# Kernel tuning notes

Hardware: AMD Instinct MI355X
Metric: run time of the kernel (lower is better)

The kernel has to match this reference:

```python
import jax, jax.numpy as jnp
import numpy as np

EPS = 1e-5

def setup_inputs() -> dict:
    key = jax.random.key(0)
    k1, k2 = jax.random.split(key)
    x = jax.random.normal(k1, (32, 256, 56, 56), dtype=jnp.float32)
    conv_w = jax.random.normal(k2, (1, 2, 5, 5), dtype=jnp.float32) * 0.1
    gamma = jnp.ones((1,), dtype=jnp.float32)
    beta = jnp.zeros((1,), dtype=jnp.float32)
    return {"x": x, "conv_w": conv_w, "gamma": gamma, "beta": beta}

def reference(x, conv_w, gamma, beta):
    # channel max and mean -> [N, 2, H, W]
    y = jnp.stack([jnp.max(x, axis=1), jnp.mean(x, axis=1)], axis=1)
    # 5x5 conv, 2->1 channels, SAME padding, no bias -> [N, 1, H, W]
    y = jax.lax.conv_general_dilated(
        y, conv_w, window_strides=(1, 1), padding=((2, 2), (2, 2)),
        dimension_numbers=("NCHW", "OIHW", "NCHW"))
    # BatchNorm2d(1) in training mode: batch statistics over (N, H, W)
    mean = jnp.mean(y, axis=(0, 2, 3), keepdims=True)
    var = jnp.mean(jnp.square(y - mean), axis=(0, 2, 3), keepdims=True)
    y = (y - mean) * jax.lax.rsqrt(var + EPS)
    y = y * gamma.reshape(1, -1, 1, 1) + beta.reshape(1, -1, 1, 1)
    # double sigmoid gate, broadcast over channels
    return x * jax.nn.sigmoid(jax.nn.sigmoid(y))
```

## Files before the change

kernel.cpp:

```cpp
#include <hip/hip_runtime.h>

#define NN 32
#define CC 256
#define HH 56
#define WW 56
#define HWSZ 3136
#define QPP 784
#define NQ 25088
#define NHW 100352
#define CBLKS 32
#define APPLY_THREADS (NQ * CBLKS)

typedef float v4f __attribute__((ext_vector_type(4)));

__device__ __forceinline__ float4 f4max(float4 a, float4 b) {
    float4 r;
    r.x = fmaxf(a.x, b.x); r.y = fmaxf(a.y, b.y);
    r.z = fmaxf(a.z, b.z); r.w = fmaxf(a.w, b.w);
    return r;
}
__device__ __forceinline__ float4 f4add(float4 a, float4 b) {
    float4 r;
    r.x = a.x + b.x; r.y = a.y + b.y; r.z = a.z + b.z; r.w = a.w + b.w;
    return r;
}

__global__ __launch_bounds__(256) void k_pool_part(const float* __restrict__ x,
                                                   float* __restrict__ pmaxp,
                                                   float* __restrict__ psump,
                                                   float* __restrict__ stats) {
    if (blockIdx.x == 0 && threadIdx.x == 0 && threadIdx.y == 0) {
        stats[0] = 0.f;
        stats[1] = 0.f;
    }
    const int tx = threadIdx.x;
    const int ty = threadIdx.y;
    const int tile = blockIdx.x >> 2;
    const int quarter = blockIdx.x & 3;
    const int qid = tile * 64 + tx;
    const int n = qid / QPP;
    const int hwq = qid - n * QPP;
    const int cbase = quarter * 64 + ty * 16;

    const float4* p = (const float4*)x + (size_t)(n * CC + cbase) * QPP + hwq;
    float4 v0 = p[0];
    float4 vmax = v0, vsum = v0;
#pragma unroll 8
    for (int i = 1; i < 16; ++i) {
        float4 v = p[(size_t)i * QPP];
        vmax = f4max(vmax, v);
        vsum = f4add(vsum, v);
    }
    __shared__ float4 smax[4][64];
    __shared__ float4 ssum[4][64];
    smax[ty][tx] = vmax;
    ssum[ty][tx] = vsum;
    __syncthreads();
    if (ty == 0) {
        float4 m = smax[0][tx];
        float4 s = ssum[0][tx];
#pragma unroll
        for (int g = 1; g < 4; ++g) {
            m = f4max(m, smax[g][tx]);
            s = f4add(s, ssum[g][tx]);
        }
        ((float4*)pmaxp)[(size_t)quarter * NQ + qid] = m;
        ((float4*)psump)[(size_t)quarter * NQ + qid] = s;
    }
}

__global__ __launch_bounds__(256) void k_merge(const float* __restrict__ pmaxp,
                                               const float* __restrict__ psump,
                                               float* __restrict__ pool) {
    const int q = blockIdx.x * 256 + threadIdx.x;
    if (q >= NQ) return;
    float4 m = ((const float4*)pmaxp)[q];
    float4 s = ((const float4*)psump)[q];
#pragma unroll
    for (int g = 1; g < 4; ++g) {
        m = f4max(m, ((const float4*)pmaxp)[(size_t)g * NQ + q]);
        s = f4add(s, ((const float4*)psump)[(size_t)g * NQ + q]);
    }
    const int n = q / QPP;
    const int hwq = q - n * QPP;
    ((float4*)pool)[(size_t)n * 2 * QPP + hwq] = m;
    float4 mean;
    mean.x = s.x * 0.00390625f; mean.y = s.y * 0.00390625f;
    mean.z = s.z * 0.00390625f; mean.w = s.w * 0.00390625f;
    ((float4*)pool)[(size_t)n * 2 * QPP + QPP + hwq] = mean;
}

__global__ __launch_bounds__(256) void k_conv(const float* __restrict__ pool,
                                              const float* __restrict__ cw,
                                              float* __restrict__ conv,
                                              float* __restrict__ stats) {
    __shared__ float w[50];
    const int tid = threadIdx.x;
    if (tid < 50) w[tid] = cw[tid];
    __syncthreads();

    const int gid = blockIdx.x * 256 + tid;
    const int n = gid / HWSZ;
    const int hw = gid - n * HWSZ;
    const int h = hw / WW;
    const int wc = hw - h * WW;

    const float* pb = pool + (size_t)n * 2 * HWSZ;
    float acc = 0.f;
#pragma unroll
    for (int ci = 0; ci < 2; ++ci)
#pragma unroll
        for (int kh = 0; kh < 5; ++kh) {
            const int hh = h + kh - 2;
            if (hh < 0 || hh >= HH) continue;
#pragma unroll
            for (int kw = 0; kw < 5; ++kw) {
                const int wwc = wc + kw - 2;
                if (wwc < 0 || wwc >= WW) continue;
                acc += pb[ci * HWSZ + hh * WW + wwc] * w[ci * 25 + kh * 5 + kw];
            }
        }
    conv[gid] = acc;

    float s = acc, s2 = acc * acc;
#pragma unroll
    for (int i = 1; i < 64; i <<= 1) {
        s += __shfl_xor(s, i);
        s2 += __shfl_xor(s2, i);
    }
    if ((tid & 63) == 0) {
        atomicAdd(&stats[0], s);
        atomicAdd(&stats[1], s2);
    }
}

__global__ __launch_bounds__(256) void k_apply(const float* __restrict__ x,
                                               const float* __restrict__ conv,
                                               const float* __restrict__ stats,
                                               const float* __restrict__ gamma,
                                               const float* __restrict__ beta,
                                               float* __restrict__ out) {
    const float invM = 1.f / (float)NHW;
    const float mean = stats[0] * invM;
    const float var = stats[1] * invM - mean * mean;
    const float scale = rsqrtf(var + 1e-5f) * gamma[0];
    const float shift = beta[0] - mean * scale;

    const int gid = blockIdx.x * 256 + threadIdx.x;
    const int v = gid / QPP;
    const int hwq = gid - v * QPP;
    const int cblk = v & (CBLKS - 1);
    const int n = v >> 5;

    const float4 cv = ((const float4*)conv)[n * QPP + hwq];
    float4 g;
    {
        float t = cv.x * scale + shift;
        float s1 = 1.f / (1.f + __expf(-t));
        g.x = 1.f / (1.f + __expf(-s1));
    }
    {
        float t = cv.y * scale + shift;
        float s1 = 1.f / (1.f + __expf(-t));
        g.y = 1.f / (1.f + __expf(-s1));
    }
    {
        float t = cv.z * scale + shift;
        float s1 = 1.f / (1.f + __expf(-t));
        g.z = 1.f / (1.f + __expf(-s1));
    }
    {
        float t = cv.w * scale + shift;
        float s1 = 1.f / (1.f + __expf(-t));
        g.w = 1.f / (1.f + __expf(-s1));
    }

    const float4* x4 = (const float4*)x + (size_t)(n * CC + cblk * 8) * QPP + hwq;
    v4f* o4 = (v4f*)out + (size_t)(n * CC + cblk * 8) * QPP + hwq;
#pragma unroll
    for (int i = 0; i < 8; ++i) {
        float4 xv = x4[(size_t)i * QPP];
        v4f r;
        r.x = xv.x * g.x; r.y = xv.y * g.y;
        r.z = xv.z * g.z; r.w = xv.w * g.w;
        __builtin_nontemporal_store(r, &o4[(size_t)i * QPP]);
    }
}

extern "C" void kernel_launch(void* const* d_in, const int* in_sizes, int n_in,
                              void* d_out, int out_size, void* d_ws, size_t ws_size,
                              hipStream_t stream) {
    const float* x = (const float*)d_in[0];
    const float* cw = (const float*)d_in[1];
    const float* gamma = (const float*)d_in[2];
    const float* beta = (const float*)d_in[3];
    float* out = (float*)d_out;

    float* ws = (float*)d_ws;
    float* pmaxp = ws;
    float* psump = pmaxp + (size_t)4 * NQ * 4;
    float* pool = psump + (size_t)4 * NQ * 4;
    float* conv = pool + 2 * NHW;
    float* stats = conv + NHW;

    k_pool_part<<<1568, dim3(64, 4), 0, stream>>>(x, pmaxp, psump, stats);
    k_merge<<<98, 256, 0, stream>>>(pmaxp, psump, pool);
    k_conv<<<392, 256, 0, stream>>>(pool, cw, conv, stats);
    k_apply<<<APPLY_THREADS / 256, 256, 0, stream>>>(x, conv, stats, gamma,
                                                     beta, out);
}
```

Baseline: 100.6 us.

## Drop shared-memory pool reduction; split channels into 8 groups of 32

The pooling kernel no longer does a shared-memory tree reduction. Each thread now reduces 32 channels straight to global partials, spread over 8 channel groups, and the merge kernel combines 8 partials instead of 4. The apply kernel gives each thread 32 channels instead of 8, so a quarter as many threads recompute the double-sigmoid gate. This cuts the LDS traffic, the barrier and the redundant gate math. The cost is fewer threads in flight, longer serial per-thread loops, and twice as many partial writes in the merge stage.

```diff
diff --git a/kernel.cpp b/kernel.cpp
--- a/kernel.cpp
+++ b/kernel.cpp
@@ -8,8 +8,9 @@
 #define QPP 784
 #define NQ 25088
 #define NHW 100352
-#define CBLKS 32
-#define APPLY_THREADS (NQ * CBLKS)
+#define NGRP 8
+#define CPGRP 32
+#define ABLK 8
 
 typedef float v4f __attribute__((ext_vector_type(4)));
 
@@ -25,48 +26,31 @@
     return r;
 }
 
-__global__ __launch_bounds__(256) void k_pool_part(const float* __restrict__ x,
-                                                   float* __restrict__ pmaxp,
-                                                   float* __restrict__ psump,
-                                                   float* __restrict__ stats) {
-    if (blockIdx.x == 0 && threadIdx.x == 0 && threadIdx.y == 0) {
+__global__ __launch_bounds__(256) void k_pool_lin(const float* __restrict__ x,
+                                                  float* __restrict__ pmaxp,
+                                                  float* __restrict__ psump,
+                                                  float* __restrict__ stats) {
+    if (blockIdx.x == 0 && threadIdx.x == 0) {
         stats[0] = 0.f;
         stats[1] = 0.f;
     }
-    const int tx = threadIdx.x;
-    const int ty = threadIdx.y;
-    const int tile = blockIdx.x >> 2;
-    const int quarter = blockIdx.x & 3;
-    const int qid = tile * 64 + tx;
-    const int n = qid / QPP;
-    const int hwq = qid - n * QPP;
-    const int cbase = quarter * 64 + ty * 16;
+    const int gid = blockIdx.x * 256 + threadIdx.x;
+    const int grp = gid / NQ;
+    const int r = gid - grp * NQ;
+    const int n = r / QPP;
+    const int hwq = r - n * QPP;
 
-    const float4* p = (const float4*)x + (size_t)(n * CC + cbase) * QPP + hwq;
+    const float4* p = (const float4*)x + (size_t)(n * CC + grp * CPGRP) * QPP + hwq;
     float4 v0 = p[0];
     float4 vmax = v0, vsum = v0;
 #pragma unroll 8
-    for (int i = 1; i < 16; ++i) {
+    for (int i = 1; i < CPGRP; ++i) {
         float4 v = p[(size_t)i * QPP];
         vmax = f4max(vmax, v);
         vsum = f4add(vsum, v);
     }
-    __shared__ float4 smax[4][64];
-    __shared__ float4 ssum[4][64];
-    smax[ty][tx] = vmax;
-    ssum[ty][tx] = vsum;
-    __syncthreads();
-    if (ty == 0) {
-        float4 m = smax[0][tx];
-        float4 s = ssum[0][tx];
-#pragma unroll
-        for (int g = 1; g < 4; ++g) {
-            m = f4max(m, smax[g][tx]);
-            s = f4add(s, ssum[g][tx]);
-        }
-        ((float4*)pmaxp)[(size_t)quarter * NQ + qid] = m;
-        ((float4*)psump)[(size_t)quarter * NQ + qid] = s;
-    }
+    ((float4*)pmaxp)[(size_t)grp * NQ + r] = vmax;
+    ((float4*)psump)[(size_t)grp * NQ + r] = vsum;
 }
 
 __global__ __launch_bounds__(256) void k_merge(const float* __restrict__ pmaxp,
@@ -77,7 +61,7 @@
     float4 m = ((const float4*)pmaxp)[q];
     float4 s = ((const float4*)psump)[q];
 #pragma unroll
-    for (int g = 1; g < 4; ++g) {
+    for (int g = 1; g < NGRP; ++g) {
         m = f4max(m, ((const float4*)pmaxp)[(size_t)g * NQ + q]);
         s = f4add(s, ((const float4*)psump)[(size_t)g * NQ + q]);
     }
@@ -149,8 +133,8 @@
     const int gid = blockIdx.x * 256 + threadIdx.x;
     const int v = gid / QPP;
     const int hwq = gid - v * QPP;
-    const int cblk = v & (CBLKS - 1);
-    const int n = v >> 5;
+    const int cblk = v & (ABLK - 1);
+    const int n = v >> 3;
 
     const float4 cv = ((const float4*)conv)[n * QPP + hwq];
     float4 g;
@@ -175,10 +159,10 @@
         g.w = 1.f / (1.f + __expf(-s1));
     }
 
-    const float4* x4 = (const float4*)x + (size_t)(n * CC + cblk * 8) * QPP + hwq;
-    v4f* o4 = (v4f*)out + (size_t)(n * CC + cblk * 8) * QPP + hwq;
-#pragma unroll
-    for (int i = 0; i < 8; ++i) {
+    const float4* x4 = (const float4*)x + (size_t)(n * CC + cblk * 32) * QPP + hwq;
+    v4f* o4 = (v4f*)out + (size_t)(n * CC + cblk * 32) * QPP + hwq;
+#pragma unroll 8
+    for (int i = 0; i < 32; ++i) {
         float4 xv = x4[(size_t)i * QPP];
         v4f r;
         r.x = xv.x * g.x; r.y = xv.y * g.y;
@@ -198,14 +182,14 @@
 
     float* ws = (float*)d_ws;
     float* pmaxp = ws;
-    float* psump = pmaxp + (size_t)4 * NQ * 4;
-    float* pool = psump + (size_t)4 * NQ * 4;
+    float* psump = pmaxp + (size_t)NGRP * NQ * 4;
+    float* pool = psump + (size_t)NGRP * NQ * 4;
     float* conv = pool + 2 * NHW;
     float* stats = conv + NHW;
 
-    k_pool_part<<<1568, dim3(64, 4), 0, stream>>>(x, pmaxp, psump, stats);
+    k_pool_lin<<<NGRP * NQ / 256, 256, 0, stream>>>(x, pmaxp, psump, stats);
     k_merge<<<98, 256, 0, stream>>>(pmaxp, psump, pool);
     k_conv<<<392, 256, 0, stream>>>(pool, cw, conv, stats);
-    k_apply<<<APPLY_THREADS / 256, 256, 0, stream>>>(x, conv, stats, gamma,
-                                                     beta, out);
+    k_apply<<<NN * ABLK * QPP / 256, 256, 0, stream>>>(x, conv, stats, gamma,
+                                                       beta, out);
 }
```

New measurement: 104.3 us. 3.7% more time.
